# Kernel tuning notes

Hardware: AMD Instinct MI355X
Metric: run time of the kernel (lower is better)

## Reference

```python
import jax, jax.numpy as jnp
import numpy as np

N = 100000
E = 1600000
IN_CH = 128
HID = 128
OUT_CH = 1
EPS = 1e-5


def setup_inputs() -> dict:
    key = jax.random.key(0)
    ks = jax.random.split(key, 20)
    x = jax.random.normal(ks[0], (N, IN_CH), dtype=jnp.float32)
    edge_index = jax.random.randint(ks[1], (2, E), 0, N, dtype=jnp.int64)

    def lin(k, fi, fo):
        k1, k2 = jax.random.split(k)
        s = 1.0 / np.sqrt(fi)
        W = jax.random.uniform(k1, (fi, fo), jnp.float32, -s, s)
        b = jax.random.uniform(k2, (fo,), jnp.float32, -s, s)
        return W, b

    W1, b1 = lin(ks[2], IN_CH, HID)
    W2, b2 = lin(ks[3], HID, HID)
    Wf1, bf1 = lin(ks[4], HID, HID)
    Wf2, bf2 = lin(ks[5], HID, HID)
    Wo, bo = lin(ks[6], HID, OUT_CH)

    def bn(k):
        k1, k2, k3, k4 = jax.random.split(k, 4)
        gamma = 1.0 + 0.1 * jax.random.normal(k1, (HID,), jnp.float32)
        beta = 0.1 * jax.random.normal(k2, (HID,), jnp.float32)
        mean = 0.1 * jax.random.normal(k3, (HID,), jnp.float32)
        var = 0.5 + jax.random.uniform(k4, (HID,), jnp.float32)
        return gamma, beta, mean, var

    g1, be1, m1, v1 = bn(ks[7])
    g2, be2, m2, v2 = bn(ks[8])
    g3, be3, m3, v3 = bn(ks[9])

    return dict(x=x, edge_index=edge_index,
                W1=W1, b1=b1, W2=W2, b2=b2,
                Wf1=Wf1, bf1=bf1, Wf2=Wf2, bf2=bf2, Wo=Wo, bo=bo,
                g1=g1, be1=be1, m1=m1, v1=v1,
                g2=g2, be2=be2, m2=m2, v2=v2,
                g3=g3, be3=be3, m3=m3, v3=v3)


def _gcn_conv(x, W, b, src, dst):
    # PyG GCNConv: add self-loops, symmetric normalization deg^-1/2 A deg^-1/2.
    loop = jnp.arange(N, dtype=src.dtype)
    s = jnp.concatenate([src, loop])   # [E+N]
    d = jnp.concatenate([dst, loop])   # [E+N]
    deg = jax.ops.segment_sum(jnp.ones(s.shape[0], x.dtype), d, num_segments=N)
    dinv = jnp.where(deg > 0, jax.lax.rsqrt(deg), 0.0)
    h = x @ W                          # [N, out]
    norm = (dinv[s] * dinv[d])[:, None]  # [E+N, 1]
    msg = h[s] * norm                  # gather + scale, [E+N, out]
    out = jax.ops.segment_sum(msg, d, num_segments=N)  # scatter-add
    return out + b


def _bn(x, gamma, beta, mean, var):
    # BatchNorm1d in inference mode (dropout treated as eval/identity).
    return (x - mean) * jax.lax.rsqrt(var + EPS) * gamma + beta


def reference(x, edge_index, W1, b1, W2, b2, Wf1, bf1, Wf2, bf2, Wo, bo,
              g1, be1, m1, v1, g2, be2, m2, v2, g3, be3, m3, v3):
    src, dst = edge_index[0], edge_index[1]
    h = jax.nn.relu(_bn(_gcn_conv(x, W1, b1, src, dst), g1, be1, m1, v1))
    h = jax.nn.relu(_bn(_gcn_conv(h, W2, b2, src, dst), g2, be2, m2, v2))
    h = jax.nn.relu(_bn(h @ Wf1 + bf1, g3, be3, m3, v3))
    h1 = jax.nn.relu(h @ Wf2 + bf2)
    raw_pred = jax.nn.softplus(h1 @ Wo + bo).reshape(-1)
    return (raw_pred, h1)
```

## Files before the change

### kernel.cpp

```cpp
#include <hip/hip_runtime.h>
#include <math.h>

#define EPS_BN 1e-5f
#define MAXNB 512

typedef __attribute__((ext_vector_type(8))) short bf16x8;
typedef __attribute__((ext_vector_type(4))) float f32x4;
typedef __attribute__((ext_vector_type(2))) float f32x2;

__device__ __forceinline__ ushort f2bf(float f) {
    uint u = __float_as_uint(f);
    u += 0x7FFF + ((u >> 16) & 1);
    return (ushort)(u >> 16);
}

__device__ __forceinline__ void gload_lds16(const void* g, void* l) {
    __builtin_amdgcn_global_load_lds((const unsigned int*)g, (unsigned int*)l, 16, 0, 0);
}

#define SWZ(row, byte_in_row) ((byte_in_row) ^ (((row) & 7) << 4))

__global__ __launch_bounds__(256) void prep_k(const float* __restrict__ W1,
                                              const float* __restrict__ W2,
                                              const float* __restrict__ W3,
                                              const float* __restrict__ W4,
                                              ushort* __restrict__ T1,
                                              ushort* __restrict__ T2,
                                              ushort* __restrict__ T3,
                                              ushort* __restrict__ T4,
                                              int* __restrict__ bcur, int NB, int stride,
                                              const float* __restrict__ b1,
                                              const float* __restrict__ g1,
                                              const float* __restrict__ be1,
                                              const float* __restrict__ m1,
                                              const float* __restrict__ v1,
                                              const float* __restrict__ b2,
                                              const float* __restrict__ g2,
                                              const float* __restrict__ be2,
                                              const float* __restrict__ m2,
                                              const float* __restrict__ v2,
                                              const float* __restrict__ b3,
                                              const float* __restrict__ g3,
                                              const float* __restrict__ be3,
                                              const float* __restrict__ m3,
                                              const float* __restrict__ v3,
                                              float* __restrict__ bnc) {
    if (blockIdx.x == 256) {
        for (int i = threadIdx.x; i < NB; i += 256) bcur[i] = i * stride;
        int cc = threadIdx.x & 127;
        int l2 = threadIdx.x >> 7;
        {
            const float* gg = l2 ? g2 : g1;
            const float* bb = l2 ? be2 : be1;
            const float* mm = l2 ? m2 : m1;
            const float* vv = l2 ? v2 : v1;
            const float* bi = l2 ? b2 : b1;
            float s = gg[cc] * rsqrtf(vv[cc] + EPS_BN);
            float* o = bnc + l2 * 256;
            o[cc] = s;
            o[128 + cc] = bb[cc] + (bi[cc] - mm[cc]) * s;
        }
        if (threadIdx.x < 128) {
            float s = g3[cc] * rsqrtf(v3[cc] + EPS_BN);
            bnc[512 + cc] = s;
            bnc[640 + cc] = be3[cc] + (b3[cc] - m3[cc]) * s;
        }
        return;
    }
    int which = blockIdx.x >> 6;
    const float* W = (which == 0) ? W1 : (which == 1) ? W2 : (which == 2) ? W3 : W4;
    ushort* T = (which == 0) ? T1 : (which == 1) ? T2 : (which == 2) ? T3 : T4;
    int i = (blockIdx.x & 63) * 256 + threadIdx.x;
    int n = i >> 7, k = i & 127;
    int idx = n & 63;
    int nperm = (n & 64) | ((idx & 3) << 4) | (idx >> 2);
    uint boff = ((uint)nperm << 8) + SWZ(nperm, (uint)k * 2);
    *(ushort*)((char*)T + boff) = f2bf(W[k * 128 + n]);
}

__global__ __launch_bounds__(256) void bucketA_k(const int* __restrict__ src,
                                                 const int* __restrict__ dst,
                                                 int* __restrict__ bcur,
                                                 int* __restrict__ coarse, int nE, int NB) {
    __shared__ int cnt[MAXNB];
    __shared__ int basix[MAXNB];
    const int tid = threadIdx.x;
    for (int i = tid; i < NB; i += 256) cnt[i] = 0;
    __syncthreads();
    int base = blockIdx.x * 4096;
    int es[16], ed[16], rk[16];
#pragma unroll
    for (int i = 0; i < 16; i++) {
        int e = base + i * 256 + tid;
        if (e < nE) {
            es[i] = src[e];
            ed[i] = dst[e];
            rk[i] = atomicAdd(&cnt[ed[i] >> 8], 1);
        } else {
            ed[i] = -1;
        }
    }
    __syncthreads();
    for (int i = tid; i < NB; i += 256)
        if (cnt[i]) basix[i] = atomicAdd(&bcur[i], cnt[i]);
    __syncthreads();
#pragma unroll
    for (int i = 0; i < 16; i++) {
        if (ed[i] >= 0)
            coarse[basix[ed[i] >> 8] + rk[i]] = es[i] | ((ed[i] & 255) << 24);
    }
}

__global__ __launch_bounds__(256) void bucketB_k(const int* __restrict__ coarse,
                                                 const int* __restrict__ bcur,
                                                 int2* __restrict__ rowptr,
                                                 int* __restrict__ col,
                                                 float* __restrict__ dinv, int N,
                                                 int stride) {
    __shared__ int cnt[256];
    __shared__ int s[256];
    __shared__ int cur[256];
    const int tid = threadIdx.x;
    const int b = blockIdx.x;
    const int beg = b * stride, end = bcur[b];
    cnt[tid] = 0;
    __syncthreads();
    for (int p = beg + tid; p < end; p += 256)
        atomicAdd(&cnt[((uint)coarse[p]) >> 24], 1);
    __syncthreads();
    int c = cnt[tid];
    s[tid] = c;
    __syncthreads();
    for (int off = 1; off < 256; off <<= 1) {
        int v = (tid >= off) ? s[tid - off] : 0;
        __syncthreads();
        s[tid] += v;
        __syncthreads();
    }
    int ex = s[tid] - c;
    int node = b * 256 + tid;
    if (node < N) {
        rowptr[node] = make_int2(beg + ex, beg + ex + c);
        dinv[node] = rsqrtf((float)c + 1.0f);
    }
    cur[tid] = ex;
    __syncthreads();
    for (int p = beg + tid; p < end; p += 256) {
        int v = coarse[p];
        int r = atomicAdd(&cur[((uint)v) >> 24], 1);
        col[beg + r] = v & 0xFFFFFF;
    }
}

__device__ __forceinline__ void add8p(f32x2* acc, uint2 a) {
    acc[0] += __builtin_amdgcn_cvt_pk_f32_fp8(a.x, false);
    acc[1] += __builtin_amdgcn_cvt_pk_f32_fp8(a.x, true);
    acc[2] += __builtin_amdgcn_cvt_pk_f32_fp8(a.y, false);
    acc[3] += __builtin_amdgcn_cvt_pk_f32_fp8(a.y, true);
}

__global__ __launch_bounds__(256) void gather_k(const unsigned char* __restrict__ h8,
                                                const int2* __restrict__ rowptr,
                                                const int* __restrict__ col,
                                                const float* __restrict__ dinv,
                                                const float* __restrict__ sc,
                                                const float* __restrict__ sh,
                                                ushort* __restrict__ out, int n) {
    int node = blockIdx.x * 4 + (threadIdx.x >> 6);
    if (node >= n) return;
    int lane = threadIdx.x & 63;
    int grp = lane >> 4;
    int li = lane & 15;
    const uint c = (uint)(li * 8);
    const uint c2 = c + (uint)(grp * 2);

    int2 rp = rowptr[node];
    float dd = dinv[node];
    f32x2 s2 = *(const f32x2*)(sc + c2);
    f32x2 h2 = *(const f32x2*)(sh + c2);

    int beg = rp.x, end = rp.y;
    int deg = end - beg;
    int nfull = deg >> 4;

    f32x2 acc[4];
#pragma unroll
    for (int j = 0; j < 4; j++) acc[j] = (f32x2){0.f, 0.f};

    if (grp == 0) {
        uint2 rv = *(const uint2*)(h8 + (((uint)node << 7) | c));
        add8p(acc, rv);
    }

    int pt = beg + grp + (nfull << 4);
    bool v0 = pt < end, v1 = pt + 4 < end, v2 = pt + 8 < end, v3 = pt + 12 < end;
    int t0 = v0 ? __builtin_nontemporal_load(col + pt) : node;
    int t1 = v1 ? __builtin_nontemporal_load(col + pt + 4) : node;
    int t2 = v2 ? __builtin_nontemporal_load(col + pt + 8) : node;
    int t3 = v3 ? __builtin_nontemporal_load(col + pt + 12) : node;

    int p = beg + grp;
    for (int it = 0; it < nfull; ++it, p += 16) {
        int s0 = __builtin_nontemporal_load(col + p);
        int s1 = __builtin_nontemporal_load(col + p + 4);
        int s2i = __builtin_nontemporal_load(col + p + 8);
        int s3 = __builtin_nontemporal_load(col + p + 12);
        uint2 a0 = *(const uint2*)(h8 + (((uint)s0 << 7) | c));
        uint2 a1 = *(const uint2*)(h8 + (((uint)s1 << 7) | c));
        uint2 a2 = *(const uint2*)(h8 + (((uint)s2i << 7) | c));
        uint2 a3 = *(const uint2*)(h8 + (((uint)s3 << 7) | c));
        add8p(acc, a0);
        add8p(acc, a1);
        add8p(acc, a2);
        add8p(acc, a3);
    }
    {
        uint2 a0 = *(const uint2*)(h8 + (((uint)t0 << 7) | c));
        uint2 a1 = *(const uint2*)(h8 + (((uint)t1 << 7) | c));
        uint2 a2 = *(const uint2*)(h8 + (((uint)t2 << 7) | c));
        uint2 a3 = *(const uint2*)(h8 + (((uint)t3 << 7) | c));
        if (!v0) { a0.x = 0u; a0.y = 0u; }
        if (!v1) { a1.x = 0u; a1.y = 0u; }
        if (!v2) { a2.x = 0u; a2.y = 0u; }
        if (!v3) { a3.x = 0u; a3.y = 0u; }
        add8p(acc, a0);
        add8p(acc, a1);
        add8p(acc, a2);
        add8p(acc, a3);
    }
#pragma unroll
    for (int j = 0; j < 4; j++) {
        f32x2 t;
        t.x = __shfl_xor(acc[j].x, 16, 64);
        t.y = __shfl_xor(acc[j].y, 16, 64);
        acc[j] += t;
        t.x = __shfl_xor(acc[j].x, 32, 64);
        t.y = __shfl_xor(acc[j].y, 32, 64);
        acc[j] += t;
    }
    f32x2 pr = (grp == 0) ? acc[0] : (grp == 1) ? acc[1] : (grp == 2) ? acc[2] : acc[3];
    float o0 = fmaxf(fmaf(pr.x * dd, s2.x, h2.x), 0.0f);
    float o1 = fmaxf(fmaf(pr.y * dd, s2.y, h2.y), 0.0f);
    uint r = (uint)f2bf(o0) | ((uint)f2bf(o1) << 16);
    uint boff = ((uint)node << 8) + SWZ((uint)node, c2 * 2);
    *(uint*)((char*)out + boff) = r;
}

template <int MODE, int F32IN>
__global__ __launch_bounds__(256) void mfma_gemm_k(const void* __restrict__ Xin,
                                                   const ushort* __restrict__ Wt,
                                                   const float* __restrict__ dinvp,
                                                   const float* __restrict__ bias,
                                                   const float* __restrict__ scp,
                                                   const float* __restrict__ shp,
                                                   const float* __restrict__ Wo,
                                                   const float* __restrict__ bo,
                                                   float* __restrict__ pred,
                                                   void* __restrict__ Y, int nrows) {
    __shared__ ushort sX[64 * 128];
    __shared__ ushort sW[128 * 128];
    __shared__ float red[64];
    const int tid = threadIdx.x;
    const int row0 = blockIdx.x * 64;
    const int wave = tid >> 6, lane = tid & 63;

    {
        const char* gW = (const char*)Wt;
#pragma unroll
        for (int i = 0; i < 8; i++) {
            int base = (wave * 8 + i) * 1024;
            gload_lds16(gW + base + lane * 16, (char*)sW + base);
        }
    }
    if (F32IN) {
        const float* Xf = (const float*)Xin;
#pragma unroll
        for (int i = 0; i < 8; i++) {
            int cidx = tid + i * 256;
            int r = cidx >> 5, o = cidx & 31;
            int rg = row0 + r;
            if (rg >= nrows) rg = nrows - 1;
            float4 v = *(const float4*)&Xf[(size_t)rg * 128 + o * 4];
            ushort4 u = {f2bf(v.x), f2bf(v.y), f2bf(v.z), f2bf(v.w)};
            *(ushort4*)((char*)sX + (r << 8) + SWZ(r, o * 8)) = u;
        }
    } else {
        const char* gX = (const char*)Xin;
#pragma unroll
        for (int i = 0; i < 4; i++) {
            int base = (wave * 4 + i) * 1024;
            int off = base + lane * 16;
            int rg = row0 + (off >> 8);
            if (rg >= nrows) rg = nrows - 1;
            gload_lds16(gX + (size_t)rg * 256 + (off & 255), (char*)sX + base);
        }
    }
    if (MODE == 2 && tid < 64) red[tid] = 0.0f;
    __syncthreads();

    const int rw = (wave >> 1) * 32;
    const int cw = (wave & 1) * 64;
    const int lm = lane & 15, lq = lane >> 4;

    f32x4 acc[2][4];
#pragma unroll
    for (int tr = 0; tr < 2; tr++)
#pragma unroll
        for (int tc = 0; tc < 4; tc++) acc[tr][tc] = (f32x4){0.f, 0.f, 0.f, 0.f};

#pragma unroll
    for (int ks = 0; ks < 4; ks++) {
        int kbyte = ks * 64 + lq * 16;
        bf16x8 a[2], b[4];
#pragma unroll
        for (int tr = 0; tr < 2; tr++) {
            int r = rw + tr * 16 + lm;
            a[tr] = *(bf16x8*)((char*)sX + (r << 8) + SWZ(r, kbyte));
        }
#pragma unroll
        for (int tc = 0; tc < 4; tc++) {
            int r = cw + tc * 16 + lm;
            b[tc] = *(bf16x8*)((char*)sW + (r << 8) + SWZ(r, kbyte));
        }
#pragma unroll
        for (int tr = 0; tr < 2; tr++)
#pragma unroll
            for (int tc = 0; tc < 4; tc++)
                acc[tr][tc] = __builtin_amdgcn_mfma_f32_16x16x32_bf16(a[tr], b[tc],
                                                                      acc[tr][tc], 0, 0, 0);
    }

    const int c0 = cw + (lm << 2);
    float psc[4], psh[4], woc[4];
#pragma unroll
    for (int tc = 0; tc < 4; tc++) {
        int c = c0 + tc;
        if (MODE == 1) {
            psc[tc] = scp[c];
            psh[tc] = shp[c];
        } else if (MODE == 2) {
            psh[tc] = bias[c];
            woc[tc] = Wo[c];
        }
    }
    float part[8];
    if (MODE == 2) {
#pragma unroll
        for (int i = 0; i < 8; i++) part[i] = 0.0f;
    }
#pragma unroll
    for (int tr = 0; tr < 2; tr++) {
#pragma unroll
        for (int r = 0; r < 4; r++) {
            int row = row0 + rw + tr * 16 + lq * 4 + r;
            if (row >= nrows) continue;
            if (MODE == 0) {
                float dd = dinvp[row];
                uint q = __builtin_amdgcn_cvt_pk_fp8_f32(acc[tr][0][r] * dd,
                                                         acc[tr][1][r] * dd, 0u, false);
                q = __builtin_amdgcn_cvt_pk_fp8_f32(acc[tr][2][r] * dd,
                                                    acc[tr][3][r] * dd, q, true);
                *(uint*)((unsigned char*)Y + (size_t)row * 128 + c0) = q;
            } else if (MODE == 1) {
                float o0 = fmaxf(fmaf(acc[tr][0][r], psc[0], psh[0]), 0.0f);
                float o1 = fmaxf(fmaf(acc[tr][1][r], psc[1], psh[1]), 0.0f);
                float o2 = fmaxf(fmaf(acc[tr][2][r], psc[2], psh[2]), 0.0f);
                float o3 = fmaxf(fmaf(acc[tr][3][r], psc[3], psh[3]), 0.0f);
                uint2 st;
                st.x = (uint)f2bf(o0) | ((uint)f2bf(o1) << 16);
                st.y = (uint)f2bf(o2) | ((uint)f2bf(o3) << 16);
                uint boff = ((uint)row << 8) + SWZ((uint)row, (uint)(c0 * 2));
                *(uint2*)((char*)Y + boff) = st;
            } else {
                float o0 = fmaxf(acc[tr][0][r] + psh[0], 0.0f);
                float o1 = fmaxf(acc[tr][1][r] + psh[1], 0.0f);
                float o2 = fmaxf(acc[tr][2][r] + psh[2], 0.0f);
                float o3 = fmaxf(acc[tr][3][r] + psh[3], 0.0f);
                float4 st = {o0, o1, o2, o3};
                *(float4*)((float*)Y + (size_t)row * 128 + c0) = st;
                part[tr * 4 + r] = fmaf(o0, woc[0],
                                   fmaf(o1, woc[1],
                                   fmaf(o2, woc[2],
                                   fmaf(o3, woc[3], part[tr * 4 + r]))));
            }
        }
    }
    if (MODE == 2) {
#pragma unroll
        for (int tr = 0; tr < 2; tr++)
#pragma unroll
            for (int r = 0; r < 4; r++) {
                int lrow = rw + tr * 16 + lq * 4 + r;
                atomicAdd(&red[lrow], part[tr * 4 + r]);
            }
        __syncthreads();
        if (tid < 64) {
            int row = row0 + tid;
            if (row < nrows) {
                float xv = red[tid] + bo[0];
                pred[row] = fmaxf(xv, 0.0f) + log1pf(expf(-fabsf(xv)));
            }
        }
    }
}

extern "C" void kernel_launch(void* const* d_in, const int* in_sizes, int n_in,
                              void* d_out, int out_size, void* d_ws, size_t ws_size,
                              hipStream_t stream) {
    const float* x = (const float*)d_in[0];
    const int* ei = (const int*)d_in[1];
    const int N = in_sizes[0] / 128;
    const int E = in_sizes[1] / 2;
    const int* srcv = ei;
    const int* dstv = ei + E;
    const float* W1 = (const float*)d_in[2];  const float* b1 = (const float*)d_in[3];
    const float* W2 = (const float*)d_in[4];  const float* b2 = (const float*)d_in[5];
    const float* Wf1 = (const float*)d_in[6]; const float* bf1 = (const float*)d_in[7];
    const float* Wf2 = (const float*)d_in[8]; const float* bf2 = (const float*)d_in[9];
    const float* Wo = (const float*)d_in[10]; const float* bo = (const float*)d_in[11];
    const float* g1 = (const float*)d_in[12], *be1 = (const float*)d_in[13],
               *m1 = (const float*)d_in[14], *v1 = (const float*)d_in[15];
    const float* g2 = (const float*)d_in[16], *be2 = (const float*)d_in[17],
               *m2 = (const float*)d_in[18], *v2 = (const float*)d_in[19];
    const float* g3 = (const float*)d_in[20], *be3 = (const float*)d_in[21],
               *m3 = (const float*)d_in[22], *v3 = (const float*)d_in[23];

    char* ws = (char*)d_ws;
    size_t off = 0;
    auto carve = [&](size_t bytes) {
        char* p = ws + off;
        off = (off + bytes + 255) & ~(size_t)255;
        return p;
    };
    const int NB = (N + 255) >> 8;
    const int STRIDE = ((E / NB + 511) + 255) & ~255;
    int* bcur = (int*)carve((size_t)MAXNB * 4);
    int2* rowptr = (int2*)carve((size_t)N * 8);
    int* col = (int*)carve((size_t)NB * STRIDE * 4);
    int* coarse = (int*)carve((size_t)NB * STRIDE * 4);
    float* dinv = (float*)carve((size_t)N * 4);
    unsigned char* bufA8 = (unsigned char*)carve((size_t)N * 128 + 16384);
    ushort* bufB = (ushort*)carve((size_t)N * 128 * 2 + 16384);
    ushort* bufC = (ushort*)carve((size_t)N * 128 * 2 + 16384);
    ushort* Wt1 = (ushort*)carve(128 * 128 * 2);
    ushort* Wt2 = (ushort*)carve(128 * 128 * 2);
    ushort* Wtf1 = (ushort*)carve(128 * 128 * 2);
    ushort* Wtf2 = (ushort*)carve(128 * 128 * 2);
    float* bnc = (float*)carve(768 * 4);

    float* out_pred = (float*)d_out;
    float* out_h1 = out_pred + N;

    const int gblocks = (N + 63) / 64;
    const int tblocks = (E + 4095) / 4096;
    const int wblocks = (N + 3) / 4;

    prep_k<<<257, 256, 0, stream>>>(W1, W2, Wf1, Wf2, Wt1, Wt2, Wtf1, Wtf2, bcur, NB,
                                    STRIDE, b1, g1, be1, m1, v1, b2, g2, be2, m2, v2,
                                    bf1, g3, be3, m3, v3, bnc);
    bucketA_k<<<tblocks, 256, 0, stream>>>(srcv, dstv, bcur, coarse, E, NB);
    bucketB_k<<<NB, 256, 0, stream>>>(coarse, bcur, rowptr, col, dinv, N, STRIDE);

    mfma_gemm_k<0, 1><<<gblocks, 256, 0, stream>>>(x, Wt1, dinv, nullptr, nullptr,
                                                   nullptr, nullptr, nullptr, nullptr,
                                                   bufA8, N);
    gather_k<<<wblocks, 256, 0, stream>>>(bufA8, rowptr, col, dinv,
                                          bnc, bnc + 128, bufB, N);
    mfma_gemm_k<0, 0><<<gblocks, 256, 0, stream>>>(bufB, Wt2, dinv, nullptr, nullptr,
                                                   nullptr, nullptr, nullptr, nullptr,
                                                   bufA8, N);
    gather_k<<<wblocks, 256, 0, stream>>>(bufA8, rowptr, col, dinv,
                                          bnc + 256, bnc + 384, bufB, N);
    mfma_gemm_k<1, 0><<<gblocks, 256, 0, stream>>>(bufB, Wtf1, nullptr, nullptr,
                                                   bnc + 512, bnc + 640, nullptr,
                                                   nullptr, nullptr, bufC, N);
    mfma_gemm_k<2, 0><<<gblocks, 256, 0, stream>>>(bufC, Wtf2, nullptr, bf2, nullptr,
                                                   nullptr, Wo, bo,
                                                   out_pred, out_h1, N);
}
```

Before: 334.4 us.

## Hold GEMM weights in registers and process two 64-row tiles per block

The MFMA GEMM kernel now loads its weight fragments straight from global memory into registers, in a plain unswizzled layout, instead of staging them in LDS. Each block handles 128 rows as two 64-row LDS tiles, and the second tile's async load overlaps compute on the first. The final-layer h1 output uses nontemporal stores. The aim is to cut LDS traffic and per-block weight reloads, at the cost of higher register pressure (launch bounds now request 3 blocks) and half as many blocks.

```diff
diff --git a/kernel.cpp b/kernel.cpp
--- a/kernel.cpp
+++ b/kernel.cpp
@@ -74,8 +74,7 @@
     int n = i >> 7, k = i & 127;
     int idx = n & 63;
     int nperm = (n & 64) | ((idx & 3) << 4) | (idx >> 2);
-    uint boff = ((uint)nperm << 8) + SWZ(nperm, (uint)k * 2);
-    *(ushort*)((char*)T + boff) = f2bf(W[k * 128 + n]);
+    T[nperm * 128 + k] = f2bf(W[k * 128 + n]);
 }
 
 __global__ __launch_bounds__(256) void bucketA_k(const int* __restrict__ src,
@@ -247,154 +246,171 @@
 }
 
 template <int MODE, int F32IN>
-__global__ __launch_bounds__(256) void mfma_gemm_k(const void* __restrict__ Xin,
-                                                   const ushort* __restrict__ Wt,
-                                                   const float* __restrict__ dinvp,
-                                                   const float* __restrict__ bias,
-                                                   const float* __restrict__ scp,
-                                                   const float* __restrict__ shp,
-                                                   const float* __restrict__ Wo,
-                                                   const float* __restrict__ bo,
-                                                   float* __restrict__ pred,
-                                                   void* __restrict__ Y, int nrows) {
-    __shared__ ushort sX[64 * 128];
-    __shared__ ushort sW[128 * 128];
-    __shared__ float red[64];
+__global__ __launch_bounds__(256, 3) void mfma_gemm_k(const void* __restrict__ Xin,
+                                                      const ushort* __restrict__ Wt,
+                                                      const float* __restrict__ dinvp,
+                                                      const float* __restrict__ bias,
+                                                      const float* __restrict__ scp,
+                                                      const float* __restrict__ shp,
+                                                      const float* __restrict__ Wo,
+                                                      const float* __restrict__ bo,
+                                                      float* __restrict__ pred,
+                                                      void* __restrict__ Y, int nrows) {
+    __shared__ ushort sX0[64 * 128];
+    __shared__ ushort sX1[64 * 128];
+    __shared__ float red[128];
     const int tid = threadIdx.x;
-    const int row0 = blockIdx.x * 64;
+    const int row0 = blockIdx.x * 128;
     const int wave = tid >> 6, lane = tid & 63;
-
-    {
-        const char* gW = (const char*)Wt;
-#pragma unroll
-        for (int i = 0; i < 8; i++) {
-            int base = (wave * 8 + i) * 1024;
-            gload_lds16(gW + base + lane * 16, (char*)sW + base);
-        }
-    }
-    if (F32IN) {
-        const float* Xf = (const float*)Xin;
-#pragma unroll
-        for (int i = 0; i < 8; i++) {
-            int cidx = tid + i * 256;
-            int r = cidx >> 5, o = cidx & 31;
-            int rg = row0 + r;
-            if (rg >= nrows) rg = nrows - 1;
-            float4 v = *(const float4*)&Xf[(size_t)rg * 128 + o * 4];
-            ushort4 u = {f2bf(v.x), f2bf(v.y), f2bf(v.z), f2bf(v.w)};
-            *(ushort4*)((char*)sX + (r << 8) + SWZ(r, o * 8)) = u;
-        }
-    } else {
-        const char* gX = (const char*)Xin;
-#pragma unroll
-        for (int i = 0; i < 4; i++) {
-            int base = (wave * 4 + i) * 1024;
-            int off = base + lane * 16;
-            int rg = row0 + (off >> 8);
-            if (rg >= nrows) rg = nrows - 1;
-            gload_lds16(gX + (size_t)rg * 256 + (off & 255), (char*)sX + base);
-        }
-    }
-    if (MODE == 2 && tid < 64) red[tid] = 0.0f;
-    __syncthreads();
-
     const int rw = (wave >> 1) * 32;
     const int cw = (wave & 1) * 64;
     const int lm = lane & 15, lq = lane >> 4;
 
-    f32x4 acc[2][4];
-#pragma unroll
-    for (int tr = 0; tr < 2; tr++)
-#pragma unroll
-        for (int tc = 0; tc < 4; tc++) acc[tr][tc] = (f32x4){0.f, 0.f, 0.f, 0.f};
-
-#pragma unroll
-    for (int ks = 0; ks < 4; ks++) {
-        int kbyte = ks * 64 + lq * 16;
-        bf16x8 a[2], b[4];
-#pragma unroll
-        for (int tr = 0; tr < 2; tr++) {
-            int r = rw + tr * 16 + lm;
-            a[tr] = *(bf16x8*)((char*)sX + (r << 8) + SWZ(r, kbyte));
-        }
-#pragma unroll
-        for (int tc = 0; tc < 4; tc++) {
-            int r = cw + tc * 16 + lm;
-            b[tc] = *(bf16x8*)((char*)sW + (r << 8) + SWZ(r, kbyte));
-        }
-#pragma unroll
-        for (int tr = 0; tr < 2; tr++)
-#pragma unroll
-            for (int tc = 0; tc < 4; tc++)
-                acc[tr][tc] = __builtin_amdgcn_mfma_f32_16x16x32_bf16(a[tr], b[tc],
-                                                                      acc[tr][tc], 0, 0, 0);
+    bf16x8 b[4][4];
+    const char* Wb = (const char*)Wt;
+#pragma unroll
+    for (int tc = 0; tc < 4; tc++) {
+        const char* rp = Wb + (cw + tc * 16 + lm) * 256;
+#pragma unroll
+        for (int ks = 0; ks < 4; ks++)
+            b[tc][ks] = *(const bf16x8*)(rp + ks * 64 + lq * 16);
+    }
+
+    if (F32IN) {
+        const float* Xf = (const float*)Xin;
+#pragma unroll
+        for (int i = 0; i < 8; i++) {
+            int chunk = i * 256 + tid;
+            int r = chunk >> 4;
+            int cb = (chunk & 15) * 16;
+            int rg = row0 + r;
+            if (rg >= nrows) rg = nrows - 1;
+            const float* rp = &Xf[(size_t)rg * 128 + cb / 2];
+            float4 v0 = *(const float4*)rp;
+            float4 v1 = *(const float4*)(rp + 4);
+            union { bf16x8 v; ushort u[8]; } t;
+            t.u[0] = f2bf(v0.x); t.u[1] = f2bf(v0.y);
+            t.u[2] = f2bf(v0.z); t.u[3] = f2bf(v0.w);
+            t.u[4] = f2bf(v1.x); t.u[5] = f2bf(v1.y);
+            t.u[6] = f2bf(v1.z); t.u[7] = f2bf(v1.w);
+            char* base = (r < 64) ? (char*)sX0 : (char*)sX1;
+            int rl = r & 63;
+            *(bf16x8*)(base + (rl << 8) + SWZ(rl, cb)) = t.v;
+        }
+    } else {
+        const char* gX = (const char*)Xin;
+#pragma unroll
+        for (int i = 0; i < 4; i++) {
+            int off = wave * 4096 + i * 1024 + lane * 16;
+            int rg = row0 + (off >> 8);
+            if (rg >= nrows) rg = nrows - 1;
+            gload_lds16(gX + (size_t)rg * 256 + (off & 255), (char*)sX0 + off);
+        }
+    }
+    if (MODE == 2 && tid < 128) red[tid] = 0.0f;
+    __syncthreads();
+
+    if (!F32IN) {
+        const char* gX = (const char*)Xin;
+#pragma unroll
+        for (int i = 0; i < 4; i++) {
+            int off = wave * 4096 + i * 1024 + lane * 16;
+            int rg = row0 + 64 + (off >> 8);
+            if (rg >= nrows) rg = nrows - 1;
+            gload_lds16(gX + (size_t)rg * 256 + (off & 255), (char*)sX1 + off);
+        }
     }
 
     const int c0 = cw + (lm << 2);
     float psc[4], psh[4], woc[4];
-#pragma unroll
-    for (int tc = 0; tc < 4; tc++) {
-        int c = c0 + tc;
-        if (MODE == 1) {
-            psc[tc] = scp[c];
-            psh[tc] = shp[c];
-        } else if (MODE == 2) {
-            psh[tc] = bias[c];
-            woc[tc] = Wo[c];
-        }
-    }
-    float part[8];
+    if (MODE == 1) {
+#pragma unroll
+        for (int tc = 0; tc < 4; tc++) { psc[tc] = scp[c0 + tc]; psh[tc] = shp[c0 + tc]; }
+    } else if (MODE == 2) {
+#pragma unroll
+        for (int tc = 0; tc < 4; tc++) { psh[tc] = bias[c0 + tc]; woc[tc] = Wo[c0 + tc]; }
+    }
+
+    auto compute = [&](const ushort* sX, int sbase) {
+        f32x4 acc[2][4];
+#pragma unroll
+        for (int tr = 0; tr < 2; tr++)
+#pragma unroll
+            for (int tc = 0; tc < 4; tc++) acc[tr][tc] = (f32x4){0.f, 0.f, 0.f, 0.f};
+#pragma unroll
+        for (int ks = 0; ks < 4; ks++) {
+            int kbyte = ks * 64 + lq * 16;
+            int r0 = rw + lm, r1 = rw + 16 + lm;
+            bf16x8 a0 = *(const bf16x8*)((const char*)sX + (r0 << 8) + SWZ(r0, kbyte));
+            bf16x8 a1 = *(const bf16x8*)((const char*)sX + (r1 << 8) + SWZ(r1, kbyte));
+#pragma unroll
+            for (int tc = 0; tc < 4; tc++) {
+                acc[0][tc] = __builtin_amdgcn_mfma_f32_16x16x32_bf16(a0, b[tc][ks],
+                                                                     acc[0][tc], 0, 0, 0);
+                acc[1][tc] = __builtin_amdgcn_mfma_f32_16x16x32_bf16(a1, b[tc][ks],
+                                                                     acc[1][tc], 0, 0, 0);
+            }
+        }
+        float part[8];
+        if (MODE == 2) {
+#pragma unroll
+            for (int i = 0; i < 8; i++) part[i] = 0.0f;
+        }
+#pragma unroll
+        for (int tr = 0; tr < 2; tr++) {
+#pragma unroll
+            for (int r = 0; r < 4; r++) {
+                int lrow = sbase + rw + tr * 16 + lq * 4 + r;
+                int row = row0 + lrow;
+                if (row >= nrows) continue;
+                if (MODE == 0) {
+                    float dd = dinvp[row];
+                    uint q = __builtin_amdgcn_cvt_pk_fp8_f32(acc[tr][0][r] * dd,
+                                                             acc[tr][1][r] * dd, 0u, false);
+                    q = __builtin_amdgcn_cvt_pk_fp8_f32(acc[tr][2][r] * dd,
+                                                        acc[tr][3][r] * dd, q, true);
+                    *(uint*)((unsigned char*)Y + (size_t)row * 128 + c0) = q;
+                } else if (MODE == 1) {
+                    float o0 = fmaxf(fmaf(acc[tr][0][r], psc[0], psh[0]), 0.0f);
+                    float o1 = fmaxf(fmaf(acc[tr][1][r], psc[1], psh[1]), 0.0f);
+                    float o2 = fmaxf(fmaf(acc[tr][2][r], psc[2], psh[2]), 0.0f);
+                    float o3 = fmaxf(fmaf(acc[tr][3][r], psc[3], psh[3]), 0.0f);
+                    uint2 st;
+                    st.x = (uint)f2bf(o0) | ((uint)f2bf(o1) << 16);
+                    st.y = (uint)f2bf(o2) | ((uint)f2bf(o3) << 16);
+                    uint boff = ((uint)row << 8) + SWZ((uint)row, (uint)(c0 * 2));
+                    *(uint2*)((char*)Y + boff) = st;
+                } else {
+                    float o0 = fmaxf(acc[tr][0][r] + psh[0], 0.0f);
+                    float o1 = fmaxf(acc[tr][1][r] + psh[1], 0.0f);
+                    float o2 = fmaxf(acc[tr][2][r] + psh[2], 0.0f);
+                    float o3 = fmaxf(acc[tr][3][r] + psh[3], 0.0f);
+                    f32x4 st = {o0, o1, o2, o3};
+                    __builtin_nontemporal_store(st,
+                        (f32x4*)((float*)Y + (size_t)row * 128 + c0));
+                    part[tr * 4 + r] = fmaf(o0, woc[0],
+                                       fmaf(o1, woc[1],
+                                       fmaf(o2, woc[2],
+                                       fmaf(o3, woc[3], part[tr * 4 + r]))));
+                }
+            }
+        }
+        if (MODE == 2) {
+#pragma unroll
+            for (int tr = 0; tr < 2; tr++)
+#pragma unroll
+                for (int r = 0; r < 4; r++)
+                    atomicAdd(&red[sbase + rw + tr * 16 + lq * 4 + r], part[tr * 4 + r]);
+        }
+    };
+
+    compute(sX0, 0);
+    __syncthreads();
+    compute(sX1, 64);
+
     if (MODE == 2) {
-#pragma unroll
-        for (int i = 0; i < 8; i++) part[i] = 0.0f;
-    }
-#pragma unroll
-    for (int tr = 0; tr < 2; tr++) {
-#pragma unroll
-        for (int r = 0; r < 4; r++) {
-            int row = row0 + rw + tr * 16 + lq * 4 + r;
-            if (row >= nrows) continue;
-            if (MODE == 0) {
-                float dd = dinvp[row];
-                uint q = __builtin_amdgcn_cvt_pk_fp8_f32(acc[tr][0][r] * dd,
-                                                         acc[tr][1][r] * dd, 0u, false);
-                q = __builtin_amdgcn_cvt_pk_fp8_f32(acc[tr][2][r] * dd,
-                                                    acc[tr][3][r] * dd, q, true);
-                *(uint*)((unsigned char*)Y + (size_t)row * 128 + c0) = q;
-            } else if (MODE == 1) {
-                float o0 = fmaxf(fmaf(acc[tr][0][r], psc[0], psh[0]), 0.0f);
-                float o1 = fmaxf(fmaf(acc[tr][1][r], psc[1], psh[1]), 0.0f);
-                float o2 = fmaxf(fmaf(acc[tr][2][r], psc[2], psh[2]), 0.0f);
-                float o3 = fmaxf(fmaf(acc[tr][3][r], psc[3], psh[3]), 0.0f);
-                uint2 st;
-                st.x = (uint)f2bf(o0) | ((uint)f2bf(o1) << 16);
-                st.y = (uint)f2bf(o2) | ((uint)f2bf(o3) << 16);
-                uint boff = ((uint)row << 8) + SWZ((uint)row, (uint)(c0 * 2));
-                *(uint2*)((char*)Y + boff) = st;
-            } else {
-                float o0 = fmaxf(acc[tr][0][r] + psh[0], 0.0f);
-                float o1 = fmaxf(acc[tr][1][r] + psh[1], 0.0f);
-                float o2 = fmaxf(acc[tr][2][r] + psh[2], 0.0f);
-                float o3 = fmaxf(acc[tr][3][r] + psh[3], 0.0f);
-                float4 st = {o0, o1, o2, o3};
-                *(float4*)((float*)Y + (size_t)row * 128 + c0) = st;
-                part[tr * 4 + r] = fmaf(o0, woc[0],
-                                   fmaf(o1, woc[1],
-                                   fmaf(o2, woc[2],
-                                   fmaf(o3, woc[3], part[tr * 4 + r]))));
-            }
-        }
-    }
-    if (MODE == 2) {
-#pragma unroll
-        for (int tr = 0; tr < 2; tr++)
-#pragma unroll
-            for (int r = 0; r < 4; r++) {
-                int lrow = rw + tr * 16 + lq * 4 + r;
-                atomicAdd(&red[lrow], part[tr * 4 + r]);
-            }
         __syncthreads();
-        if (tid < 64) {
+        if (tid < 128) {
             int row = row0 + tid;
             if (row < nrows) {
                 float xv = red[tid] + bo[0];
@@ -440,8 +456,8 @@
     int* coarse = (int*)carve((size_t)NB * STRIDE * 4);
     float* dinv = (float*)carve((size_t)N * 4);
     unsigned char* bufA8 = (unsigned char*)carve((size_t)N * 128 + 16384);
-    ushort* bufB = (ushort*)carve((size_t)N * 128 * 2 + 16384);
-    ushort* bufC = (ushort*)carve((size_t)N * 128 * 2 + 16384);
+    ushort* bufB = (ushort*)carve((size_t)N * 128 * 2 + 32768);
+    ushort* bufC = (ushort*)carve((size_t)N * 128 * 2 + 32768);
     ushort* Wt1 = (ushort*)carve(128 * 128 * 2);
     ushort* Wt2 = (ushort*)carve(128 * 128 * 2);
     ushort* Wtf1 = (ushort*)carve(128 * 128 * 2);
@@ -451,7 +467,7 @@
     float* out_pred = (float*)d_out;
     float* out_h1 = out_pred + N;
 
-    const int gblocks = (N + 63) / 64;
+    const int gblocks = (N + 127) / 128;
     const int tblocks = (E + 4095) / 4096;
     const int wblocks = (N + 3) / 4;
 
```

New measurement: 362.2 us. 8.3% more time.

## Fuse the two trailing MLP GEMMs into one kernel keeping intermediate in LDS

Applied to the files above, without the earlier changes.

Merges the Wf1 (BN+ReLU) GEMM and the Wf2 (bias+ReLU+output head) GEMM into a single kernel. The intermediate bf16 activations are written back into shared memory instead of going to a global buffer, so a full N x 128 write and reread and one launch are avoided. The h1 output is also written with nontemporal stores. The trade-off is extra LDS reloading of the second weight matrix inside each block and additional syncthreads barriers.

```diff
diff --git a/kernel.cpp b/kernel.cpp
--- a/kernel.cpp
+++ b/kernel.cpp
@@ -250,41 +250,123 @@
 __global__ __launch_bounds__(256) void mfma_gemm_k(const void* __restrict__ Xin,
                                                    const ushort* __restrict__ Wt,
                                                    const float* __restrict__ dinvp,
-                                                   const float* __restrict__ bias,
-                                                   const float* __restrict__ scp,
-                                                   const float* __restrict__ shp,
-                                                   const float* __restrict__ Wo,
-                                                   const float* __restrict__ bo,
-                                                   float* __restrict__ pred,
                                                    void* __restrict__ Y, int nrows) {
+    __shared__ ushort sX[64 * 128];
+    __shared__ ushort sW[128 * 128];
+    const int tid = threadIdx.x;
+    const int row0 = blockIdx.x * 64;
+    const int wave = tid >> 6, lane = tid & 63;
+
+    {
+        const char* gW = (const char*)Wt;
+#pragma unroll
+        for (int i = 0; i < 8; i++) {
+            int base = (wave * 8 + i) * 1024;
+            gload_lds16(gW + base + lane * 16, (char*)sW + base);
+        }
+    }
+    if (F32IN) {
+        const float* Xf = (const float*)Xin;
+#pragma unroll
+        for (int i = 0; i < 8; i++) {
+            int cidx = tid + i * 256;
+            int r = cidx >> 5, o = cidx & 31;
+            int rg = row0 + r;
+            if (rg >= nrows) rg = nrows - 1;
+            float4 v = *(const float4*)&((const float*)Xin)[(size_t)rg * 128 + o * 4];
+            ushort4 u = {f2bf(v.x), f2bf(v.y), f2bf(v.z), f2bf(v.w)};
+            *(ushort4*)((char*)sX + (r << 8) + SWZ(r, o * 8)) = u;
+        }
+    } else {
+        const char* gX = (const char*)Xin;
+#pragma unroll
+        for (int i = 0; i < 4; i++) {
+            int base = (wave * 4 + i) * 1024;
+            int off = base + lane * 16;
+            int rg = row0 + (off >> 8);
+            if (rg >= nrows) rg = nrows - 1;
+            gload_lds16(gX + (size_t)rg * 256 + (off & 255), (char*)sX + base);
+        }
+    }
+    __syncthreads();
+
+    const int rw = ((tid >> 6) >> 1) * 32;
+    const int cw = ((tid >> 6) & 1) * 64;
+    const int lm = lane & 15, lq = lane >> 4;
+
+    f32x4 acc[2][4];
+#pragma unroll
+    for (int tr = 0; tr < 2; tr++)
+#pragma unroll
+        for (int tc = 0; tc < 4; tc++) acc[tr][tc] = (f32x4){0.f, 0.f, 0.f, 0.f};
+
+#pragma unroll
+    for (int ks = 0; ks < 4; ks++) {
+        int kbyte = ks * 64 + lq * 16;
+        bf16x8 a[2], b[4];
+#pragma unroll
+        for (int tr = 0; tr < 2; tr++) {
+            int r = rw + tr * 16 + lm;
+            a[tr] = *(bf16x8*)((char*)sX + (r << 8) + SWZ(r, kbyte));
+        }
+#pragma unroll
+        for (int tc = 0; tc < 4; tc++) {
+            int r = cw + tc * 16 + lm;
+            b[tc] = *(bf16x8*)((char*)sW + (r << 8) + SWZ(r, kbyte));
+        }
+#pragma unroll
+        for (int tr = 0; tr < 2; tr++)
+#pragma unroll
+            for (int tc = 0; tc < 4; tc++)
+                acc[tr][tc] = __builtin_amdgcn_mfma_f32_16x16x32_bf16(a[tr], b[tc],
+                                                                      acc[tr][tc], 0, 0, 0);
+    }
+
+    const int c0 = cw + (lm << 2);
+#pragma unroll
+    for (int tr = 0; tr < 2; tr++) {
+#pragma unroll
+        for (int r = 0; r < 4; r++) {
+            int row = row0 + rw + tr * 16 + lq * 4 + r;
+            if (row >= nrows) continue;
+            float dd = dinvp[row];
+            uint q = __builtin_amdgcn_cvt_pk_fp8_f32(acc[tr][0][r] * dd,
+                                                     acc[tr][1][r] * dd, 0u, false);
+            q = __builtin_amdgcn_cvt_pk_fp8_f32(acc[tr][2][r] * dd,
+                                                acc[tr][3][r] * dd, q, true);
+            *(uint*)((unsigned char*)Y + (size_t)row * 128 + c0) = q;
+        }
+    }
+}
+
+__global__ __launch_bounds__(256) void gemm34_k(const ushort* __restrict__ Xin,
+                                                const ushort* __restrict__ Wt3,
+                                                const ushort* __restrict__ Wt4,
+                                                const float* __restrict__ sc3,
+                                                const float* __restrict__ sh3,
+                                                const float* __restrict__ bias4,
+                                                const float* __restrict__ Wo,
+                                                const float* __restrict__ bo,
+                                                float* __restrict__ pred,
+                                                float* __restrict__ Y, int nrows) {
     __shared__ ushort sX[64 * 128];
     __shared__ ushort sW[128 * 128];
     __shared__ float red[64];
     const int tid = threadIdx.x;
     const int row0 = blockIdx.x * 64;
     const int wave = tid >> 6, lane = tid & 63;
+    const int rw = (wave >> 1) * 32;
+    const int cw = (wave & 1) * 64;
+    const int lm = lane & 15, lq = lane >> 4;
+    const int c0 = cw + (lm << 2);
 
     {
-        const char* gW = (const char*)Wt;
+        const char* gW = (const char*)Wt3;
 #pragma unroll
         for (int i = 0; i < 8; i++) {
             int base = (wave * 8 + i) * 1024;
             gload_lds16(gW + base + lane * 16, (char*)sW + base);
         }
-    }
-    if (F32IN) {
-        const float* Xf = (const float*)Xin;
-#pragma unroll
-        for (int i = 0; i < 8; i++) {
-            int cidx = tid + i * 256;
-            int r = cidx >> 5, o = cidx & 31;
-            int rg = row0 + r;
-            if (rg >= nrows) rg = nrows - 1;
-            float4 v = *(const float4*)&Xf[(size_t)rg * 128 + o * 4];
-            ushort4 u = {f2bf(v.x), f2bf(v.y), f2bf(v.z), f2bf(v.w)};
-            *(ushort4*)((char*)sX + (r << 8) + SWZ(r, o * 8)) = u;
-        }
-    } else {
         const char* gX = (const char*)Xin;
 #pragma unroll
         for (int i = 0; i < 4; i++) {
@@ -295,19 +377,22 @@
             gload_lds16(gX + (size_t)rg * 256 + (off & 255), (char*)sX + base);
         }
     }
-    if (MODE == 2 && tid < 64) red[tid] = 0.0f;
-    __syncthreads();
-
-    const int rw = (wave >> 1) * 32;
-    const int cw = (wave & 1) * 64;
-    const int lm = lane & 15, lq = lane >> 4;
+    if (tid < 64) red[tid] = 0.0f;
+    float p3sc[4], p3sh[4], p4sh[4], woc[4];
+#pragma unroll
+    for (int tc = 0; tc < 4; tc++) {
+        p3sc[tc] = sc3[c0 + tc];
+        p3sh[tc] = sh3[c0 + tc];
+        p4sh[tc] = bias4[c0 + tc];
+        woc[tc] = Wo[c0 + tc];
+    }
+    __syncthreads();
 
     f32x4 acc[2][4];
 #pragma unroll
     for (int tr = 0; tr < 2; tr++)
 #pragma unroll
         for (int tc = 0; tc < 4; tc++) acc[tr][tc] = (f32x4){0.f, 0.f, 0.f, 0.f};
-
 #pragma unroll
     for (int ks = 0; ks < 4; ks++) {
         int kbyte = ks * 64 + lq * 16;
@@ -329,77 +414,95 @@
                 acc[tr][tc] = __builtin_amdgcn_mfma_f32_16x16x32_bf16(a[tr], b[tc],
                                                                       acc[tr][tc], 0, 0, 0);
     }
-
-    const int c0 = cw + (lm << 2);
-    float psc[4], psh[4], woc[4];
-#pragma unroll
-    for (int tc = 0; tc < 4; tc++) {
-        int c = c0 + tc;
-        if (MODE == 1) {
-            psc[tc] = scp[c];
-            psh[tc] = shp[c];
-        } else if (MODE == 2) {
-            psh[tc] = bias[c];
-            woc[tc] = Wo[c];
-        }
+    uint2 hst[2][4];
+#pragma unroll
+    for (int tr = 0; tr < 2; tr++)
+#pragma unroll
+        for (int r = 0; r < 4; r++) {
+            float o0 = fmaxf(fmaf(acc[tr][0][r], p3sc[0], p3sh[0]), 0.0f);
+            float o1 = fmaxf(fmaf(acc[tr][1][r], p3sc[1], p3sh[1]), 0.0f);
+            float o2 = fmaxf(fmaf(acc[tr][2][r], p3sc[2], p3sh[2]), 0.0f);
+            float o3 = fmaxf(fmaf(acc[tr][3][r], p3sc[3], p3sh[3]), 0.0f);
+            hst[tr][r].x = (uint)f2bf(o0) | ((uint)f2bf(o1) << 16);
+            hst[tr][r].y = (uint)f2bf(o2) | ((uint)f2bf(o3) << 16);
+        }
+    __syncthreads();
+
+#pragma unroll
+    for (int tr = 0; tr < 2; tr++)
+#pragma unroll
+        for (int r = 0; r < 4; r++) {
+            int lrow = rw + tr * 16 + lq * 4 + r;
+            *(uint2*)((char*)sX + (lrow << 8) + SWZ(lrow, (uint)(c0 * 2))) = hst[tr][r];
+        }
+    {
+        const char* gW = (const char*)Wt4;
+#pragma unroll
+        for (int i = 0; i < 8; i++) {
+            int base = (wave * 8 + i) * 1024;
+            gload_lds16(gW + base + lane * 16, (char*)sW + base);
+        }
+    }
+    __syncthreads();
+
+#pragma unroll
+    for (int tr = 0; tr < 2; tr++)
+#pragma unroll
+        for (int tc = 0; tc < 4; tc++) acc[tr][tc] = (f32x4){0.f, 0.f, 0.f, 0.f};
+#pragma unroll
+    for (int ks = 0; ks < 4; ks++) {
+        int kbyte = ks * 64 + lq * 16;
+        bf16x8 a[2], b[4];
+#pragma unroll
+        for (int tr = 0; tr < 2; tr++) {
+            int r = rw + tr * 16 + lm;
+            a[tr] = *(bf16x8*)((char*)sX + (r << 8) + SWZ(r, kbyte));
+        }
+#pragma unroll
+        for (int tc = 0; tc < 4; tc++) {
+            int r = cw + tc * 16 + lm;
+            b[tc] = *(bf16x8*)((char*)sW + (r << 8) + SWZ(r, kbyte));
+        }
+#pragma unroll
+        for (int tr = 0; tr < 2; tr++)
+#pragma unroll
+            for (int tc = 0; tc < 4; tc++)
+                acc[tr][tc] = __builtin_amdgcn_mfma_f32_16x16x32_bf16(a[tr], b[tc],
+                                                                      acc[tr][tc], 0, 0, 0);
     }
     float part[8];
-    if (MODE == 2) {
-#pragma unroll
-        for (int i = 0; i < 8; i++) part[i] = 0.0f;
-    }
+#pragma unroll
+    for (int i = 0; i < 8; i++) part[i] = 0.0f;
 #pragma unroll
     for (int tr = 0; tr < 2; tr++) {
 #pragma unroll
         for (int r = 0; r < 4; r++) {
-            int row = row0 + rw + tr * 16 + lq * 4 + r;
+            int lrow = rw + tr * 16 + lq * 4 + r;
+            int row = row0 + lrow;
             if (row >= nrows) continue;
-            if (MODE == 0) {
-                float dd = dinvp[row];
-                uint q = __builtin_amdgcn_cvt_pk_fp8_f32(acc[tr][0][r] * dd,
-                                                         acc[tr][1][r] * dd, 0u, false);
-                q = __builtin_amdgcn_cvt_pk_fp8_f32(acc[tr][2][r] * dd,
-                                                    acc[tr][3][r] * dd, q, true);
-                *(uint*)((unsigned char*)Y + (size_t)row * 128 + c0) = q;
-            } else if (MODE == 1) {
-                float o0 = fmaxf(fmaf(acc[tr][0][r], psc[0], psh[0]), 0.0f);
-                float o1 = fmaxf(fmaf(acc[tr][1][r], psc[1], psh[1]), 0.0f);
-                float o2 = fmaxf(fmaf(acc[tr][2][r], psc[2], psh[2]), 0.0f);
-                float o3 = fmaxf(fmaf(acc[tr][3][r], psc[3], psh[3]), 0.0f);
-                uint2 st;
-                st.x = (uint)f2bf(o0) | ((uint)f2bf(o1) << 16);
-                st.y = (uint)f2bf(o2) | ((uint)f2bf(o3) << 16);
-                uint boff = ((uint)row << 8) + SWZ((uint)row, (uint)(c0 * 2));
-                *(uint2*)((char*)Y + boff) = st;
-            } else {
-                float o0 = fmaxf(acc[tr][0][r] + psh[0], 0.0f);
-                float o1 = fmaxf(acc[tr][1][r] + psh[1], 0.0f);
-                float o2 = fmaxf(acc[tr][2][r] + psh[2], 0.0f);
-                float o3 = fmaxf(acc[tr][3][r] + psh[3], 0.0f);
-                float4 st = {o0, o1, o2, o3};
-                *(float4*)((float*)Y + (size_t)row * 128 + c0) = st;
-                part[tr * 4 + r] = fmaf(o0, woc[0],
-                                   fmaf(o1, woc[1],
-                                   fmaf(o2, woc[2],
-                                   fmaf(o3, woc[3], part[tr * 4 + r]))));
-            }
-        }
-    }
-    if (MODE == 2) {
-#pragma unroll
-        for (int tr = 0; tr < 2; tr++)
-#pragma unroll
-            for (int r = 0; r < 4; r++) {
-                int lrow = rw + tr * 16 + lq * 4 + r;
-                atomicAdd(&red[lrow], part[tr * 4 + r]);
-            }
-        __syncthreads();
-        if (tid < 64) {
-            int row = row0 + tid;
-            if (row < nrows) {
-                float xv = red[tid] + bo[0];
-                pred[row] = fmaxf(xv, 0.0f) + log1pf(expf(-fabsf(xv)));
-            }
+            float o0 = fmaxf(acc[tr][0][r] + p4sh[0], 0.0f);
+            float o1 = fmaxf(acc[tr][1][r] + p4sh[1], 0.0f);
+            float o2 = fmaxf(acc[tr][2][r] + p4sh[2], 0.0f);
+            float o3 = fmaxf(acc[tr][3][r] + p4sh[3], 0.0f);
+            f32x4 st = {o0, o1, o2, o3};
+            __builtin_nontemporal_store(st, (f32x4*)(Y + (size_t)row * 128 + c0));
+            part[tr * 4 + r] = fmaf(o0, woc[0],
+                               fmaf(o1, woc[1],
+                               fmaf(o2, woc[2],
+                               fmaf(o3, woc[3], part[tr * 4 + r]))));
+        }
+    }
+#pragma unroll
+    for (int tr = 0; tr < 2; tr++)
+#pragma unroll
+        for (int r = 0; r < 4; r++)
+            atomicAdd(&red[rw + tr * 16 + lq * 4 + r], part[tr * 4 + r]);
+    __syncthreads();
+    if (tid < 64) {
+        int row = row0 + tid;
+        if (row < nrows) {
+            float xv = red[tid] + bo[0];
+            pred[row] = fmaxf(xv, 0.0f) + log1pf(expf(-fabsf(xv)));
         }
     }
 }
@@ -441,7 +544,6 @@
     float* dinv = (float*)carve((size_t)N * 4);
     unsigned char* bufA8 = (unsigned char*)carve((size_t)N * 128 + 16384);
     ushort* bufB = (ushort*)carve((size_t)N * 128 * 2 + 16384);
-    ushort* bufC = (ushort*)carve((size_t)N * 128 * 2 + 16384);
     ushort* Wt1 = (ushort*)carve(128 * 128 * 2);
     ushort* Wt2 = (ushort*)carve(128 * 128 * 2);
     ushort* Wtf1 = (ushort*)carve(128 * 128 * 2);
@@ -461,20 +563,12 @@
     bucketA_k<<<tblocks, 256, 0, stream>>>(srcv, dstv, bcur, coarse, E, NB);
     bucketB_k<<<NB, 256, 0, stream>>>(coarse, bcur, rowptr, col, dinv, N, STRIDE);
 
-    mfma_gemm_k<0, 1><<<gblocks, 256, 0, stream>>>(x, Wt1, dinv, nullptr, nullptr,
-                                                   nullptr, nullptr, nullptr, nullptr,
-                                                   bufA8, N);
+    mfma_gemm_k<0, 1><<<gblocks, 256, 0, stream>>>(x, Wt1, dinv, bufA8, N);
     gather_k<<<wblocks, 256, 0, stream>>>(bufA8, rowptr, col, dinv,
                                           bnc, bnc + 128, bufB, N);
-    mfma_gemm_k<0, 0><<<gblocks, 256, 0, stream>>>(bufB, Wt2, dinv, nullptr, nullptr,
-                                                   nullptr, nullptr, nullptr, nullptr,
-                                                   bufA8, N);
+    mfma_gemm_k<0, 0><<<gblocks, 256, 0, stream>>>(bufB, Wt2, dinv, bufA8, N);
     gather_k<<<wblocks, 256, 0, stream>>>(bufA8, rowptr, col, dinv,
                                           bnc + 256, bnc + 384, bufB, N);
-    mfma_gemm_k<1, 0><<<gblocks, 256, 0, stream>>>(bufB, Wtf1, nullptr, nullptr,
-                                                   bnc + 512, bnc + 640, nullptr,
-                                                   nullptr, nullptr, bufC, N);
-    mfma_gemm_k<2, 0><<<gblocks, 256, 0, stream>>>(bufC, Wtf2, nullptr, bf2, nullptr,
-                                                   nullptr, Wo, bo,
-                                                   out_pred, out_h1, N);
-}
+    gemm34_k<<<gblocks, 256, 0, stream>>>(bufB, Wtf1, Wtf2, bnc + 512, bnc + 640,
+                                          bf2, Wo, bo, out_pred, out_h1, N);
+}
```

Result: no change. 328.1 us (-1.9%).
